# Kernel optimization log

Measured on AMD Instinct MI355X. Metric: run time of the kernel, lower is better.

The kernel has to match this reference:

```python
import jax, jax.numpy as jnp
import numpy as np
from jax import lax

B, C, H, W = 4, 512, 64, 64
C8 = C // 8
OUT = 256
BN_EPS = 1e-5


def setup_inputs() -> dict:
    key = jax.random.key(0)
    ks = jax.random.split(key, 12)
    s = lambda k, shape, fan: jax.random.normal(k, shape, jnp.float32) * (1.0 / np.sqrt(fan))
    return {
        "x": jax.random.normal(ks[0], (B, C, H, W), jnp.float32),
        "wq": s(ks[1], (C8, C), C), "bq": jnp.zeros((C8,), jnp.float32),
        "wk": s(ks[2], (C8, C), C), "bk": jnp.zeros((C8,), jnp.float32),
        "wv": s(ks[3], (C, C), C),  "bv": jnp.zeros((C,), jnp.float32),
        "ca_w1": s(ks[4], (C8, C), C),
        "ca_w2": s(ks[5], (C, C8), C8),
        "conv_w": s(ks[6], (OUT, C, 3, 3), C * 9),
        "bn_gamma": jnp.ones((OUT,), jnp.float32),
        "bn_beta": jnp.zeros((OUT,), jnp.float32),
        "bn_mean": jnp.zeros((OUT,), jnp.float32),
        "bn_var": jnp.ones((OUT,), jnp.float32),
    }


def reference(x, wq, bq, wk, bk, wv, bv, ca_w1, ca_w2, conv_w,
              bn_gamma, bn_beta, bn_mean, bn_var):
    b, c, h, w = x.shape
    n = h * w
    xf = x.reshape(b, c, n)  # [B,C,N]

    # ---- Position attention ----
    q = jnp.einsum('qc,bcn->bnq', wq, xf) + bq            # [B,N,C8]
    k = jnp.einsum('kc,bcn->bkn', wk, xf) + bk[:, None]   # [B,C8,N]
    energy = jnp.einsum('bnq,bqm->bnm', q, k)             # [B,N,N]
    attn = jax.nn.softmax(energy, axis=-1)
    v = jnp.einsum('vc,bcn->bvn', wv, xf) + bv[:, None]   # [B,C,N]
    # torch: bmm(value, attention^T) -> out[b,c,m] = sum_n v[b,c,n]*attn[b,m,n]
    pa = jnp.einsum('bcn,bmn->bcm', v, attn).reshape(b, c, h, w) + x

    # ---- Channel attention (SE-style, avg+max pooled, shared MLP) ----
    avg = jnp.mean(pa, axis=(2, 3))   # [B,C]
    mx = jnp.max(pa, axis=(2, 3))     # [B,C]
    fc = lambda z: jnp.einsum('oc,bc->bo', ca_w2,
                              jax.nn.relu(jnp.einsum('hc,bc->bh', ca_w1, z)))
    scale = jax.nn.sigmoid(fc(avg) + fc(mx))[:, :, None, None]
    ca = scale * pa

    # ---- Conv 3x3 + BN (eval mode) + ReLU ----
    y = lax.conv_general_dilated(ca, conv_w, (1, 1), 'SAME',
                                 dimension_numbers=('NCHW', 'OIHW', 'NCHW'))
    inv = lax.rsqrt(bn_var + BN_EPS)
    y = (y - bn_mean[:, None, None]) * (inv * bn_gamma)[:, None, None] + bn_beta[:, None, None]
    return jax.nn.relu(y)
```

## Files before the change

### kernel.cpp

```cpp
#include <hip/hip_runtime.h>

#define NB 4
#define CIN 512
#define NPIX 4096
#define CQK 64
#define COUT 256
#define PPIX 4356

typedef __bf16 bh16;
typedef _Float16 fh16;
typedef __attribute__((ext_vector_type(8))) __bf16 bf16x8;
typedef __attribute__((ext_vector_type(8))) _Float16 f16x8;
typedef __attribute__((ext_vector_type(16))) float f32x16;

#define AS1 __attribute__((address_space(1)))
#define AS3 __attribute__((address_space(3)))

__device__ __forceinline__ void glds16(const void* g, void* l) {
  __builtin_amdgcn_global_load_lds((const AS1 unsigned int*)g, (AS3 unsigned int*)l, 16, 0, 0);
}

__device__ __forceinline__ float fexp2(float x) {
#if __has_builtin(__builtin_amdgcn_exp2f)
  return __builtin_amdgcn_exp2f(x);
#else
  return __expf(x * 0.6931471805599453f);
#endif
}

__global__ __launch_bounds__(256) void transpose_bf_k(const float* __restrict__ src,
                                                      bh16* __restrict__ dst,
                                                      int rows, int cols) {
  __shared__ float tile[32][33];
  const int b = blockIdx.z;
  const int c0 = blockIdx.x * 32;
  const int r0 = blockIdx.y * 32;
  const float* s = src + (size_t)b * rows * cols;
  bh16* d = dst + (size_t)b * rows * cols;
  const int tx = threadIdx.x, ty = threadIdx.y;
#pragma unroll
  for (int i = 0; i < 32; i += 8)
    tile[ty + i][tx] = s[(size_t)(r0 + ty + i) * cols + (c0 + tx)];
  __syncthreads();
#pragma unroll
  for (int i = 0; i < 32; i += 8)
    d[(size_t)(c0 + ty + i) * rows + (r0 + tx)] = (bh16)tile[tx][ty + i];
}

__global__ __launch_bounds__(256) void wcast_k(const float* __restrict__ wq,
                                               const float* __restrict__ wk,
                                               const float* __restrict__ wv,
                                               const float* __restrict__ bq,
                                               const float* __restrict__ bk,
                                               bh16* __restrict__ Wqk,
                                               bh16* __restrict__ wvb,
                                               float* __restrict__ bias128) {
  const int idx = blockIdx.x * 256 + threadIdx.x;
  if (idx < 65536) {
    Wqk[idx] = (bh16)(idx < 32768 ? wq[idx] : wk[idx - 32768]);
  } else {
    const int j = idx - 65536;
    wvb[j] = (bh16)wv[j];
  }
  if (idx < 128) bias128[idx] = idx < 64 ? bq[idx] : bk[idx - 64];
}

__global__ __launch_bounds__(256) void qk_proj_k(const bh16* __restrict__ xTb,
                                                 const bh16* __restrict__ Wqk,
                                                 const float* __restrict__ bias128,
                                                 bh16* __restrict__ Qb,
                                                 bh16* __restrict__ Kf) {
  const int blk = blockIdx.x;
  const int t = threadIdx.x;
  const int w = t >> 6, l31 = t & 31, hi = (t & 63) >> 5;
  __shared__ __align__(16) bh16 As[2][64 * 64];
  f32x16 acc[2];
#pragma unroll
  for (int nt = 0; nt < 2; nt++)
#pragma unroll
    for (int r = 0; r < 16; r++) acc[nt][r] = 0.0f;

#define QK_STAGE(kc, buf)                                                           \
  {                                                                                 \
    _Pragma("unroll") for (int i = 0; i < 2; i++) {                                 \
      const int s = i * 256 + t;                                                    \
      const int n = s >> 3, slot = s & 7;                                           \
      glds16(xTb + (size_t)(blk * 64 + n) * CIN + (kc) * 64 + (((slot + n) & 7) * 8), \
             &As[buf][(size_t)(i * 256 + w * 64) * 8]);                             \
    }                                                                               \
  }

  QK_STAGE(0, 0);
  __syncthreads();
  for (int kc = 0; kc < 8; kc++) {
    if (kc < 7) QK_STAGE(kc + 1, (kc + 1) & 1);
    const bh16* as = As[kc & 1];
#pragma unroll
    for (int ks = 0; ks < 4; ks++) {
      const bf16x8 bfr = *(const bf16x8*)(Wqk + (size_t)(w * 32 + l31) * CIN + kc * 64 + ks * 16 + hi * 8);
      const int kk = ks * 2 + hi;
#pragma unroll
      for (int nt = 0; nt < 2; nt++) {
        const int n = nt * 32 + l31;
        const bf16x8 a = *(const bf16x8*)&as[(size_t)(n * 8 + ((kk - n) & 7)) * 8];
        acc[nt] = __builtin_amdgcn_mfma_f32_32x32x16_bf16(a, bfr, acc[nt], 0, 0, 0);
      }
    }
    __syncthreads();
  }
#undef QK_STAGE
  const int o = w * 32 + l31;
  const float bo = bias128[o];
  if (w < 2) {
#pragma unroll
    for (int nt = 0; nt < 2; nt++)
#pragma unroll
      for (int r = 0; r < 16; r++) {
        const int nloc = nt * 32 + (r & 3) + 8 * (r >> 2) + 4 * hi;
        Qb[(size_t)(blk * 64 + nloc) * 64 + o] = (bh16)((acc[nt][r] + bo) * 1.44269504088896f);
      }
  } else {
    const int b = blk >> 6, jtile = blk & 63;
    const int k = o - 64, kg = k >> 3, k7 = k & 7;
    bh16* kdst = Kf + (((size_t)(b * 64 + jtile) * 8 + kg) * 64) * 8 + k7;
#pragma unroll
    for (int nt = 0; nt < 2; nt++)
#pragma unroll
      for (int r = 0; r < 16; r++) {
        const int j = nt * 32 + (r & 3) + 8 * (r >> 2) + 4 * hi;
        kdst[(size_t)j * 8] = (bh16)(acc[nt][r] + bo);
      }
  }
}

__global__ __launch_bounds__(256) void v_proj_k(const bh16* __restrict__ xTb,
                                                const bh16* __restrict__ wvb,
                                                const float* __restrict__ bv,
                                                bh16* __restrict__ Vf) {
  const int nblk = blockIdx.x;
  const int cblk = blockIdx.y;
  const int b = blockIdx.z;
  const int t = threadIdx.x;
  const int w = t >> 6, l31 = t & 31, hi = (t & 63) >> 5;
  __shared__ __align__(16) bh16 Bs[2][256 * 64];
  f32x16 acc[2][2];
#pragma unroll
  for (int mt = 0; mt < 2; mt++)
#pragma unroll
    for (int nt = 0; nt < 2; nt++)
#pragma unroll
      for (int r = 0; r < 16; r++) acc[mt][nt][r] = 0.0f;

#define V_STAGE(kc, buf)                                                              \
  {                                                                                   \
    _Pragma("unroll") for (int i = 0; i < 8; i++) {                                   \
      const int s = i * 256 + t;                                                      \
      const int n = s >> 3, slot = s & 7;                                             \
      glds16(xTb + (size_t)(b * NPIX + nblk * 256 + n) * CIN + (kc) * 64 + (((slot + n) & 7) * 8), \
             &Bs[buf][(size_t)(i * 256 + w * 64) * 8]);                               \
    }                                                                                 \
  }

  V_STAGE(0, 0);
  __syncthreads();
  for (int kc = 0; kc < 8; kc++) {
    if (kc < 7) V_STAGE(kc + 1, (kc + 1) & 1);
    const bh16* bs = Bs[kc & 1];
#pragma unroll
    for (int ks = 0; ks < 4; ks++) {
      const int kk = ks * 2 + hi;
      bf16x8 a[2], bfr[2];
#pragma unroll
      for (int mt = 0; mt < 2; mt++)
        a[mt] = *(const bf16x8*)(wvb + (size_t)(cblk * 64 + mt * 32 + l31) * CIN + kc * 64 + ks * 16 + hi * 8);
#pragma unroll
      for (int nt = 0; nt < 2; nt++) {
        const int n = w * 64 + nt * 32 + l31;
        bfr[nt] = *(const bf16x8*)&bs[(size_t)(n * 8 + ((kk - n) & 7)) * 8];
      }
#pragma unroll
      for (int mt = 0; mt < 2; mt++)
#pragma unroll
        for (int nt = 0; nt < 2; nt++)
          acc[mt][nt] = __builtin_amdgcn_mfma_f32_32x32x16_bf16(a[mt], bfr[nt], acc[mt][nt], 0, 0, 0);
    }
    __syncthreads();
  }
#undef V_STAGE
  const int ntile0 = nblk * 4 + w;
#pragma unroll
  for (int mt = 0; mt < 2; mt++)
#pragma unroll
    for (int r = 0; r < 16; r++) {
      const int c = cblk * 64 + mt * 32 + (r & 3) + 8 * (r >> 2) + 4 * hi;
      const float bvc = bv[c];
#pragma unroll
      for (int nt = 0; nt < 2; nt++) {
        const int nl = nt * 32 + l31;
        Vf[(((size_t)(b * 64 + ntile0) * 8 + (nl >> 3)) * 512 + c) * 8 + (nl & 7)] =
            (bh16)(acc[mt][nt][r] + bvc);
      }
    }
}

__global__ __launch_bounds__(256, 2) void attn1p_k(const bh16* __restrict__ Qb,
                                                   const bh16* __restrict__ Kf,
                                                   const bh16* __restrict__ Vf,
                                                   const float* __restrict__ x,
                                                   float* __restrict__ pa) {
  const int id = blockIdx.x + 2 * (blockIdx.y + 64 * blockIdx.z);
  const int b = (id & 7) >> 1;
  const int cblk = id & 1;
  const int mblk = (id >> 3) * 64;
  const int t = threadIdx.x;
  const int w = t >> 6, l31 = t & 31, hi = (t >> 5) & 1;
  const int jhalf = w & 1, mhalf = w >> 1;
  __shared__ __align__(16) bh16 Ps[2][8 * 64 * 8];
  __shared__ float lred[4][32];
  __shared__ float linvL[64];

  bf16x8 qf[4];
  {
    const bh16* qrow = Qb + (size_t)(b * NPIX + mblk + mhalf * 32 + l31) * 64;
#pragma unroll
    for (int ks = 0; ks < 4; ks++) qf[ks] = *(const bf16x8*)(qrow + ks * 16 + hi * 8);
  }
  const bh16* kfb = Kf + (size_t)b * (64 * 8 * 64 * 8);
  const bh16* vfb = Vf + (size_t)b * (64 * 8 * 512 * 8);
  const int cbase = cblk * 256 + w * 64;

#define KADDR(tile, ks) (kfb + (((size_t)(tile) * 8 + (ks) * 2 + hi) * 64 + jhalf * 32 + l31) * 8)
#define VADDR(tile, ks, ct) (vfb + (((size_t)(tile) * 8 + (ks) * 2 + hi) * 512 + cbase + (ct) * 32 + l31) * 8)

  f32x16 acc[2][2];
#pragma unroll
  for (int mt = 0; mt < 2; mt++)
#pragma unroll
    for (int ct = 0; ct < 2; ct++)
#pragma unroll
      for (int r = 0; r < 16; r++) acc[mt][ct][r] = 0.0f;
  float4 lsacc;
  lsacc.x = 0.0f; lsacc.y = 0.0f; lsacc.z = 0.0f; lsacc.w = 0.0f;

  bf16x8 kf_nxt[4], kf_fly[4];
  bf16x8 vf_use[4][2], vf_rdy[4][2];
  f32x16 s1;
  {
    bf16x8 k0[4];
#pragma unroll
    for (int ks = 0; ks < 4; ks++) {
      k0[ks] = *(const bf16x8*)KADDR(0, ks);
#pragma unroll
      for (int ct = 0; ct < 2; ct++) vf_rdy[ks][ct] = *(const bf16x8*)VADDR(0, ks, ct);
    }
#pragma unroll
    for (int ks = 0; ks < 4; ks++) {
      kf_nxt[ks] = *(const bf16x8*)KADDR(1, ks);
      kf_fly[ks] = *(const bf16x8*)KADDR(2, ks);
    }
#pragma unroll
    for (int r = 0; r < 16; r++) s1[r] = 0.0f;
#pragma unroll
    for (int ks = 0; ks < 4; ks++)
      s1 = __builtin_amdgcn_mfma_f32_32x32x16_bf16(k0[ks], qf[ks], s1, 0, 0, 0);
  }

  for (int it = 0; it < 64; it++) {
    f32x16 s1n;
#pragma unroll
    for (int r = 0; r < 16; r++) s1n[r] = 0.0f;
#pragma unroll
    for (int ks = 0; ks < 4; ks++)
      s1n = __builtin_amdgcn_mfma_f32_32x32x16_bf16(kf_nxt[ks], qf[ks], s1n, 0, 0, 0);

    const bh16* ps = Ps[(it + 1) & 1];
    bh16* psw = Ps[it & 1];
    if (it) {
#pragma unroll
      for (int ks = 0; ks < 4; ks++) {
        bf16x8 pf0 = *(const bf16x8*)&ps[(size_t)((ks * 2 + hi) * 64 + l31) * 8];
        bf16x8 pf1 = *(const bf16x8*)&ps[(size_t)((ks * 2 + hi) * 64 + 32 + l31) * 8];
        acc[0][0] = __builtin_amdgcn_mfma_f32_32x32x16_bf16(pf0, vf_use[ks][0], acc[0][0], 0, 0, 0);
        acc[0][1] = __builtin_amdgcn_mfma_f32_32x32x16_bf16(pf0, vf_use[ks][1], acc[0][1], 0, 0, 0);
        {
          union { bh16 h[4]; uint2 u2; } pk;
#pragma unroll
          for (int q = 0; q < 4; q++) {
            const float p = fexp2(s1[ks * 4 + q]);
            lsacc[q] += p;
            pk.h[q] = (bh16)p;
          }
          *(uint2*)(void*)&psw[(size_t)((jhalf * 4 + ks) * 64 + mhalf * 32 + l31) * 8 + hi * 4] = pk.u2;
        }
        acc[1][0] = __builtin_amdgcn_mfma_f32_32x32x16_bf16(pf1, vf_use[ks][0], acc[1][0], 0, 0, 0);
        acc[1][1] = __builtin_amdgcn_mfma_f32_32x32x16_bf16(pf1, vf_use[ks][1], acc[1][1], 0, 0, 0);
      }
    } else {
#pragma unroll
      for (int g = 0; g < 4; g++) {
        union { bh16 h[4]; uint2 u2; } pk;
#pragma unroll
        for (int q = 0; q < 4; q++) {
          const float p = fexp2(s1[g * 4 + q]);
          lsacc[q] += p;
          pk.h[q] = (bh16)p;
        }
        *(uint2*)(void*)&psw[(size_t)((jhalf * 4 + g) * 64 + mhalf * 32 + l31) * 8 + hi * 4] = pk.u2;
      }
    }
    __syncthreads();
    s1 = s1n;
    const int kt = (it + 3 < 64) ? it + 3 : 63;
    const int vt = (it + 1 < 64) ? it + 1 : 63;
#pragma unroll
    for (int ks = 0; ks < 4; ks++) {
      kf_nxt[ks] = kf_fly[ks];
      kf_fly[ks] = *(const bf16x8*)KADDR(kt, ks);
      vf_use[ks][0] = vf_rdy[ks][0];
      vf_use[ks][1] = vf_rdy[ks][1];
      vf_rdy[ks][0] = *(const bf16x8*)VADDR(vt, ks, 0);
      vf_rdy[ks][1] = *(const bf16x8*)VADDR(vt, ks, 1);
    }
  }
  {
    const bh16* ps = Ps[1];
#pragma unroll
    for (int ks = 0; ks < 4; ks++) {
      bf16x8 pf0 = *(const bf16x8*)&ps[(size_t)((ks * 2 + hi) * 64 + l31) * 8];
      bf16x8 pf1 = *(const bf16x8*)&ps[(size_t)((ks * 2 + hi) * 64 + 32 + l31) * 8];
      acc[0][0] = __builtin_amdgcn_mfma_f32_32x32x16_bf16(pf0, vf_use[ks][0], acc[0][0], 0, 0, 0);
      acc[0][1] = __builtin_amdgcn_mfma_f32_32x32x16_bf16(pf0, vf_use[ks][1], acc[0][1], 0, 0, 0);
      acc[1][0] = __builtin_amdgcn_mfma_f32_32x32x16_bf16(pf1, vf_use[ks][0], acc[1][0], 0, 0, 0);
      acc[1][1] = __builtin_amdgcn_mfma_f32_32x32x16_bf16(pf1, vf_use[ks][1], acc[1][1], 0, 0, 0);
    }
  }
#undef KADDR
#undef VADDR

  float lsum = (lsacc.x + lsacc.y) + (lsacc.z + lsacc.w);
  lsum += __shfl_xor(lsum, 32);
  if (hi == 0) lred[w][l31] = lsum;
  __syncthreads();
  if (t < 64) linvL[t] = 1.0f / (lred[(t >> 5) * 2][t & 31] + lred[(t >> 5) * 2 + 1][t & 31]);
  __syncthreads();

#pragma unroll
  for (int mt = 0; mt < 2; mt++) {
#pragma unroll
    for (int g = 0; g < 4; g++) {
      const int mloc = mt * 32 + g * 8 + hi * 4;
      const float4 lv = *(const float4*)&linvL[mloc];
#pragma unroll
      for (int ct = 0; ct < 2; ct++) {
        const size_t base = (size_t)(b * CIN + cblk * 256 + w * 64 + ct * 32 + l31) * NPIX + mblk + mloc;
        const float4 xv = *(const float4*)&x[base];
        float4 r;
        r.x = acc[mt][ct][g * 4 + 0] * lv.x + xv.x;
        r.y = acc[mt][ct][g * 4 + 1] * lv.y + xv.y;
        r.z = acc[mt][ct][g * 4 + 2] * lv.z + xv.z;
        r.w = acc[mt][ct][g * 4 + 3] * lv.w + xv.w;
        *(float4*)&pa[base] = r;
      }
    }
  }
}

__global__ __launch_bounds__(256) void pool2_k(const float* __restrict__ pa,
                                               float* __restrict__ avgv,
                                               float* __restrict__ maxv) {
  const int t = threadIdx.x;
  const int row = blockIdx.x * 4 + (t >> 6);
  const int lane = t & 63;
  const float* base = pa + (size_t)row * NPIX;
  float s = 0.0f, mx = -1e30f;
#pragma unroll
  for (int i = 0; i < 16; i++) {
    const float4 v = *(const float4*)(base + i * 256 + lane * 4);
    s += v.x + v.y + v.z + v.w;
    mx = fmaxf(mx, fmaxf(fmaxf(v.x, v.y), fmaxf(v.z, v.w)));
  }
#pragma unroll
  for (int d = 1; d < 64; d <<= 1) {
    s += __shfl_xor(s, d);
    mx = fmaxf(mx, __shfl_xor(mx, d));
  }
  if (lane == 0) {
    avgv[row] = s * (1.0f / 4096.0f);
    maxv[row] = mx;
  }
}

__global__ __launch_bounds__(256) void mlp2_k(const float* __restrict__ avgv,
                                              const float* __restrict__ maxv,
                                              const float* __restrict__ w1,
                                              const float* __restrict__ w2,
                                              float* __restrict__ scale) {
  const int b = blockIdx.x;
  const int t = threadIdx.x;
  __shared__ float avg_l[CIN], max_l[CIN], hbuf[128];
#pragma unroll
  for (int h = 0; h < 2; h++) {
    const int c = t + h * 256;
    avg_l[c] = avgv[b * CIN + c];
    max_l[c] = maxv[b * CIN + c];
  }
  __syncthreads();
  if (t < 128) {
    const float* src = (t < 64) ? avg_l : max_l;
    const int o = t & 63;
    float sacc = 0.0f;
    for (int c = 0; c < CIN; c++) sacc += w1[o * CIN + c] * src[c];
    hbuf[t] = fmaxf(sacc, 0.0f);
  }
  __syncthreads();
#pragma unroll
  for (int h = 0; h < 2; h++) {
    const int c = t + h * 256;
    float sacc = 0.0f;
#pragma unroll
    for (int k = 0; k < 64; k++) sacc += w2[c * 64 + k] * (hbuf[k] + hbuf[64 + k]);
    scale[b * CIN + c] = 1.0f / (1.0f + __expf(-sacc));
  }
}

__global__ __launch_bounds__(256) void pack_k(const float* __restrict__ pa,
                                              const float* __restrict__ scl,
                                              fh16* __restrict__ pab) {
  __shared__ float tile[32][65];
  const int n0 = blockIdx.x * 32;
  const int c0 = blockIdx.y * 64;
  const int b = blockIdx.z;
  const int t = threadIdx.x;
  {
    const int px = t & 31, cc = t >> 5;
#pragma unroll
    for (int i = 0; i < 8; i++) {
      const int c = cc * 8 + i;
      tile[px][c] = pa[((size_t)(b * CIN + c0 + c)) * NPIX + n0 + px] * scl[b * CIN + c0 + c];
    }
  }
  __syncthreads();
  {
    const int pixr = t >> 5, c2 = (t & 31) * 2;
#pragma unroll
    for (int j = 0; j < 4; j++) {
      const int pix = pixr + j * 8;
      const int n = n0 + pix;
      const int pp = ((n >> 6) + 1) * 66 + (n & 63) + 1;
      union { fh16 h[2]; unsigned int u; } pk;
      pk.h[0] = (fh16)tile[pix][c2];
      pk.h[1] = (fh16)tile[pix][c2 + 1];
      *(unsigned int*)(void*)(pab + ((size_t)b * PPIX + pp) * CIN + c0 + c2) = pk.u;
    }
  }
}

__global__ __launch_bounds__(256) void bzero_k(fh16* __restrict__ pab) {
  const int t = threadIdx.x;
  const int p = blockIdx.x * 4 + (t >> 6);
  const int b = blockIdx.y;
  int pp;
  if (p < 66) pp = p;
  else if (p < 132) pp = 65 * 66 + (p - 66);
  else if (p < 196) pp = (p - 131) * 66;
  else pp = (p - 195) * 66 + 65;
  uint4 z = {0u, 0u, 0u, 0u};
  *(uint4*)(void*)(pab + ((size_t)b * PPIX + pp) * CIN + (t & 63) * 8) = z;
}

__global__ __launch_bounds__(256) void wpack_k(const float* __restrict__ cw,
                                               fh16* __restrict__ wp) {
  const int slot = blockIdx.x * 256 + threadIdx.x;
  const int oblk = slot / 36864;
  const int r1 = slot - oblk * 36864;
  const int chunk = r1 / 1152;
  const int r2 = r1 - chunk * 1152;
  const int tap = r2 >> 7;
  const int r3 = r2 & 127;
  const int h = r3 >> 6;
  const int o = r3 & 63;
  const size_t sbase = (size_t)(oblk * 64 + o) * 4608 + (size_t)(chunk * 16 + h * 8) * 9 + tap;
  union { fh16 h8[8]; uint4 u4; } pk;
#pragma unroll
  for (int i = 0; i < 8; i++) pk.h8[i] = (fh16)cw[sbase + (size_t)i * 9];
  *(uint4*)(void*)(wp + (size_t)slot * 8) = pk.u4;
}

__global__ __launch_bounds__(256) void conv_mfma_k(const fh16* __restrict__ pab,
                                                   const fh16* __restrict__ wp,
                                                   const float* __restrict__ gamma,
                                                   const float* __restrict__ beta,
                                                   const float* __restrict__ mean,
                                                   const float* __restrict__ var,
                                                   float* __restrict__ out) {
  const int y0 = blockIdx.x * 4;
  const int oblk = blockIdx.y;
  const int b = blockIdx.z;
  const int t = threadIdx.x;
  const int w = t >> 6, lane = t & 63, l31 = lane & 31, hi = lane >> 5;
  __shared__ __align__(16) fh16 Xs[2][416 * 16];
  __shared__ __align__(16) fh16 Ws[2][9 * 64 * 16];
  __shared__ float sb[64], bb[64];
  if (t < 64) {
    const int o = oblk * 64 + t;
    const float inv = rsqrtf(var[o] + 1e-5f);
    const float sc = inv * gamma[o];
    sb[t] = sc;
    bb[t] = beta[o] - mean[o] * sc;
  }
  f32x16 o00, o01, o10, o11;
#pragma unroll
  for (int r = 0; r < 16; r++) { o00[r] = 0.0f; o01[r] = 0.0f; o10[r] = 0.0f; o11[r] = 0.0f; }

  const fh16* xbase = pab + ((size_t)b * PPIX + y0 * 66) * CIN + (size_t)(lane & 31) * CIN + (lane >> 5) * 8;
  const fh16* wbase = wp + (size_t)oblk * 32 * 9216 + lane * 8;

#define STAGE(chunk, buf)                                                        \
  {                                                                              \
    const fh16* xs = xbase + (chunk) * 16;                                       \
    for (int i = w; i < 13; i += 4)                                              \
      glds16(xs + (size_t)i * 32 * CIN, &Xs[buf][i * 512]);                      \
    const fh16* wsrc = wbase + (size_t)(chunk) * 9216;                           \
    for (int i = w; i < 18; i += 4)                                              \
      glds16(wsrc + (size_t)i * 512, &Ws[buf][i * 512]);                         \
  }

  STAGE(0, 0);
  __syncthreads();
  for (int chunk = 0; chunk < 32; chunk++) {
    if (chunk < 31) STAGE(chunk + 1, (chunk + 1) & 1);
    const fh16* xs = Xs[chunk & 1];
    const fh16* ws = Ws[chunk & 1];
#pragma unroll
    for (int tap = 0; tap < 9; tap++) {
      const int ky = tap / 3, kx = tap - ky * 3;
      const f16x8 a0 = *(const f16x8*)&ws[tap * 1024 + hi * 512 + l31 * 8];
      const f16x8 a1 = *(const f16x8*)&ws[tap * 1024 + hi * 512 + (32 + l31) * 8];
      const int row0 = (w + ky) * 66 + l31 + kx;
      const int row1 = row0 + 32;
      const f16x8 b0 = *(const f16x8*)&xs[(row0 >> 5) * 512 + hi * 256 + (row0 & 31) * 8];
      const f16x8 b1 = *(const f16x8*)&xs[(row1 >> 5) * 512 + hi * 256 + (row1 & 31) * 8];
      o00 = __builtin_amdgcn_mfma_f32_32x32x16_f16(a0, b0, o00, 0, 0, 0);
      o01 = __builtin_amdgcn_mfma_f32_32x32x16_f16(a0, b1, o01, 0, 0, 0);
      o10 = __builtin_amdgcn_mfma_f32_32x32x16_f16(a1, b0, o10, 0, 0, 0);
      o11 = __builtin_amdgcn_mfma_f32_32x32x16_f16(a1, b1, o11, 0, 0, 0);
    }
    __syncthreads();
  }
#undef STAGE

  const f32x16* accs[2][2] = {{&o00, &o01}, {&o10, &o11}};
#pragma unroll
  for (int mt = 0; mt < 2; mt++) {
#pragma unroll
    for (int nt = 0; nt < 2; nt++) {
      const f32x16& A = *accs[mt][nt];
#pragma unroll
      for (int r = 0; r < 16; r++) {
        const int cl = mt * 32 + (r & 3) + 8 * (r >> 2) + 4 * hi;
        const int pix = nt * 32 + l31;
        const float y = A[r] * sb[cl] + bb[cl];
        out[((size_t)(b * COUT + oblk * 64 + cl)) * NPIX + (y0 + w) * 64 + pix] = fmaxf(y, 0.0f);
      }
    }
  }
}

extern "C" void kernel_launch(void* const* d_in, const int* in_sizes, int n_in,
                              void* d_out, int out_size, void* d_ws, size_t ws_size,
                              hipStream_t stream) {
  (void)in_sizes; (void)n_in; (void)out_size; (void)ws_size;
  const float* x        = (const float*)d_in[0];
  const float* wq       = (const float*)d_in[1];
  const float* bq       = (const float*)d_in[2];
  const float* wk       = (const float*)d_in[3];
  const float* bk       = (const float*)d_in[4];
  const float* wv       = (const float*)d_in[5];
  const float* bv       = (const float*)d_in[6];
  const float* ca_w1    = (const float*)d_in[7];
  const float* ca_w2    = (const float*)d_in[8];
  const float* conv_w   = (const float*)d_in[9];
  const float* bn_gamma = (const float*)d_in[10];
  const float* bn_beta  = (const float*)d_in[11];
  const float* bn_mean  = (const float*)d_in[12];
  const float* bn_var   = (const float*)d_in[13];
  float* out = (float*)d_out;

  float* ws = (float*)d_ws;
  float* pa      = ws;
  bh16*  Vf      = (bh16*)(ws + 8388608);
  fh16*  wpck    = (fh16*)(ws + 8388608);
  bh16*  Qb      = (bh16*)(ws + 12582912);
  bh16*  Kf      = (bh16*)(ws + 13107200);
  bh16*  xTb     = (bh16*)(ws + 13631488);
  fh16*  pab     = (fh16*)(ws + 13631488);
  bh16*  Wqk     = (bh16*)(ws + 17825792);
  bh16*  wvb     = (bh16*)(ws + 17858560);
  float* bias128 = ws + 17989632;
  float* avgv    = ws + 18100224;
  float* maxv    = ws + 18102272;
  float* scl     = ws + 18104320;

  wcast_k<<<dim3(1280, 1, 1), 256, 0, stream>>>(wq, wk, wv, bq, bk, Wqk, wvb, bias128);
  transpose_bf_k<<<dim3(NPIX / 32, CIN / 32, NB), dim3(32, 8, 1), 0, stream>>>(x, xTb, CIN, NPIX);
  qk_proj_k<<<dim3(256, 1, 1), 256, 0, stream>>>(xTb, Wqk, bias128, Qb, Kf);
  v_proj_k<<<dim3(16, 8, NB), 256, 0, stream>>>(xTb, wvb, bv, Vf);
  attn1p_k<<<dim3(2, 64, NB), 256, 0, stream>>>(Qb, Kf, Vf, x, pa);
  bzero_k<<<dim3(65, NB, 1), 256, 0, stream>>>(pab);
  pool2_k<<<dim3(512, 1, 1), 256, 0, stream>>>(pa, avgv, maxv);
  mlp2_k<<<dim3(NB, 1, 1), 256, 0, stream>>>(avgv, maxv, ca_w1, ca_w2, scl);
  pack_k<<<dim3(NPIX / 32, CIN / 64, NB), 256, 0, stream>>>(pa, scl, pab);
  wpack_k<<<dim3(576, 1, 1), 256, 0, stream>>>(conv_w, wpck);
  conv_mfma_k<<<dim3(16, 4, NB), 256, 0, stream>>>(pab, wpck, bn_gamma, bn_beta,
                                                   bn_mean, bn_var, out);
}
```

Measured before the change: 335.3 us.

## Fuse channel pooling into attention epilogue and store pa as fp16 NHWC

The attention kernel now writes pa as fp16 in pixel-major (NHWC) layout and computes per-block partial sums and maxima per channel. This removes the separate pool2 kernel, and the MLP kernel reduces the 64 partials instead. The pack kernel becomes a simple scaled copy with no shared-memory transpose. The K/V prefetch pipeline is also made shallower to lower register pressure. In exchange, the epilogue now issues scattered 2-byte stores, and the pre-scale activation is rounded to fp16.

```diff
diff --git a/kernel.cpp b/kernel.cpp
--- a/kernel.cpp
+++ b/kernel.cpp
@@ -207,7 +207,9 @@
                                                    const bh16* __restrict__ Kf,
                                                    const bh16* __restrict__ Vf,
                                                    const float* __restrict__ x,
-                                                   float* __restrict__ pa) {
+                                                   fh16* __restrict__ pa,
+                                                   float* __restrict__ psum,
+                                                   float* __restrict__ pmax) {
   const int id = blockIdx.x + 2 * (blockIdx.y + 64 * blockIdx.z);
   const int b = (id & 7) >> 1;
   const int cblk = id & 1;
@@ -242,8 +244,8 @@
   float4 lsacc;
   lsacc.x = 0.0f; lsacc.y = 0.0f; lsacc.z = 0.0f; lsacc.w = 0.0f;
 
-  bf16x8 kf_nxt[4], kf_fly[4];
-  bf16x8 vf_use[4][2], vf_rdy[4][2];
+  bf16x8 kf_nxt[4];
+  bf16x8 vf_use[4][2];
   f32x16 s1;
   {
     bf16x8 k0[4];
@@ -251,13 +253,10 @@
     for (int ks = 0; ks < 4; ks++) {
       k0[ks] = *(const bf16x8*)KADDR(0, ks);
 #pragma unroll
-      for (int ct = 0; ct < 2; ct++) vf_rdy[ks][ct] = *(const bf16x8*)VADDR(0, ks, ct);
-    }
-#pragma unroll
-    for (int ks = 0; ks < 4; ks++) {
-      kf_nxt[ks] = *(const bf16x8*)KADDR(1, ks);
-      kf_fly[ks] = *(const bf16x8*)KADDR(2, ks);
-    }
+      for (int ct = 0; ct < 2; ct++) vf_use[ks][ct] = *(const bf16x8*)VADDR(0, ks, ct);
+    }
+#pragma unroll
+    for (int ks = 0; ks < 4; ks++) kf_nxt[ks] = *(const bf16x8*)KADDR(1, ks);
 #pragma unroll
     for (int r = 0; r < 16; r++) s1[r] = 0.0f;
 #pragma unroll
@@ -272,6 +271,11 @@
 #pragma unroll
     for (int ks = 0; ks < 4; ks++)
       s1n = __builtin_amdgcn_mfma_f32_32x32x16_bf16(kf_nxt[ks], qf[ks], s1n, 0, 0, 0);
+    {
+      const int kt = (it + 2 < 64) ? it + 2 : 63;
+#pragma unroll
+      for (int ks = 0; ks < 4; ks++) kf_nxt[ks] = *(const bf16x8*)KADDR(kt, ks);
+    }
 
     const bh16* ps = Ps[(it + 1) & 1];
     bh16* psw = Ps[it & 1];
@@ -294,6 +298,8 @@
         }
         acc[1][0] = __builtin_amdgcn_mfma_f32_32x32x16_bf16(pf1, vf_use[ks][0], acc[1][0], 0, 0, 0);
         acc[1][1] = __builtin_amdgcn_mfma_f32_32x32x16_bf16(pf1, vf_use[ks][1], acc[1][1], 0, 0, 0);
+        vf_use[ks][0] = *(const bf16x8*)VADDR(it, ks, 0);
+        vf_use[ks][1] = *(const bf16x8*)VADDR(it, ks, 1);
       }
     } else {
 #pragma unroll
@@ -310,17 +316,6 @@
     }
     __syncthreads();
     s1 = s1n;
-    const int kt = (it + 3 < 64) ? it + 3 : 63;
-    const int vt = (it + 1 < 64) ? it + 1 : 63;
-#pragma unroll
-    for (int ks = 0; ks < 4; ks++) {
-      kf_nxt[ks] = kf_fly[ks];
-      kf_fly[ks] = *(const bf16x8*)KADDR(kt, ks);
-      vf_use[ks][0] = vf_rdy[ks][0];
-      vf_use[ks][1] = vf_rdy[ks][1];
-      vf_rdy[ks][0] = *(const bf16x8*)VADDR(vt, ks, 0);
-      vf_rdy[ks][1] = *(const bf16x8*)VADDR(vt, ks, 1);
-    }
   }
   {
     const bh16* ps = Ps[1];
@@ -344,6 +339,8 @@
   if (t < 64) linvL[t] = 1.0f / (lred[(t >> 5) * 2][t & 31] + lred[(t >> 5) * 2 + 1][t & 31]);
   __syncthreads();
 
+  float csum[2] = {0.0f, 0.0f};
+  float cmax[2] = {-1e30f, -1e30f};
 #pragma unroll
   for (int mt = 0; mt < 2; mt++) {
 #pragma unroll
@@ -352,46 +349,40 @@
       const float4 lv = *(const float4*)&linvL[mloc];
 #pragma unroll
       for (int ct = 0; ct < 2; ct++) {
-        const size_t base = (size_t)(b * CIN + cblk * 256 + w * 64 + ct * 32 + l31) * NPIX + mblk + mloc;
-        const float4 xv = *(const float4*)&x[base];
-        float4 r;
-        r.x = acc[mt][ct][g * 4 + 0] * lv.x + xv.x;
-        r.y = acc[mt][ct][g * 4 + 1] * lv.y + xv.y;
-        r.z = acc[mt][ct][g * 4 + 2] * lv.z + xv.z;
-        r.w = acc[mt][ct][g * 4 + 3] * lv.w + xv.w;
-        *(float4*)&pa[base] = r;
-      }
-    }
-  }
-}
-
-__global__ __launch_bounds__(256) void pool2_k(const float* __restrict__ pa,
-                                               float* __restrict__ avgv,
-                                               float* __restrict__ maxv) {
-  const int t = threadIdx.x;
-  const int row = blockIdx.x * 4 + (t >> 6);
-  const int lane = t & 63;
-  const float* base = pa + (size_t)row * NPIX;
-  float s = 0.0f, mx = -1e30f;
-#pragma unroll
-  for (int i = 0; i < 16; i++) {
-    const float4 v = *(const float4*)(base + i * 256 + lane * 4);
-    s += v.x + v.y + v.z + v.w;
-    mx = fmaxf(mx, fmaxf(fmaxf(v.x, v.y), fmaxf(v.z, v.w)));
-  }
-#pragma unroll
-  for (int d = 1; d < 64; d <<= 1) {
-    s += __shfl_xor(s, d);
-    mx = fmaxf(mx, __shfl_xor(mx, d));
-  }
-  if (lane == 0) {
-    avgv[row] = s * (1.0f / 4096.0f);
-    maxv[row] = mx;
-  }
-}
-
-__global__ __launch_bounds__(256) void mlp2_k(const float* __restrict__ avgv,
-                                              const float* __restrict__ maxv,
+        const int c = cbase + ct * 32 + l31;
+        const float4 xv = *(const float4*)&x[(size_t)(b * CIN + c) * NPIX + mblk + mloc];
+        float r0 = acc[mt][ct][g * 4 + 0] * lv.x + xv.x;
+        float r1 = acc[mt][ct][g * 4 + 1] * lv.y + xv.y;
+        float r2 = acc[mt][ct][g * 4 + 2] * lv.z + xv.z;
+        float r3 = acc[mt][ct][g * 4 + 3] * lv.w + xv.w;
+        csum[ct] += (r0 + r1) + (r2 + r3);
+        cmax[ct] = fmaxf(cmax[ct], fmaxf(fmaxf(r0, r1), fmaxf(r2, r3)));
+        fh16* pd = pa + ((size_t)(b * NPIX) + mblk + mloc) * CIN + c;
+        pd[0 * CIN] = (fh16)r0;
+        pd[1 * CIN] = (fh16)r1;
+        pd[2 * CIN] = (fh16)r2;
+        pd[3 * CIN] = (fh16)r3;
+      }
+    }
+  }
+#pragma unroll
+  for (int ct = 0; ct < 2; ct++) {
+    csum[ct] += __shfl_xor(csum[ct], 32);
+    cmax[ct] = fmaxf(cmax[ct], __shfl_xor(cmax[ct], 32));
+  }
+  if (hi == 0) {
+    const int mb = mblk >> 6;
+#pragma unroll
+    for (int ct = 0; ct < 2; ct++) {
+      const int c = cbase + ct * 32 + l31;
+      psum[((size_t)b * 64 + mb) * CIN + c] = csum[ct];
+      pmax[((size_t)b * 64 + mb) * CIN + c] = cmax[ct];
+    }
+  }
+}
+
+__global__ __launch_bounds__(256) void mlp2_k(const float* __restrict__ psum,
+                                              const float* __restrict__ pmax,
                                               const float* __restrict__ w1,
                                               const float* __restrict__ w2,
                                               float* __restrict__ scale) {
@@ -401,8 +392,14 @@
 #pragma unroll
   for (int h = 0; h < 2; h++) {
     const int c = t + h * 256;
-    avg_l[c] = avgv[b * CIN + c];
-    max_l[c] = maxv[b * CIN + c];
+    float s = 0.0f, m = -1e30f;
+#pragma unroll
+    for (int k = 0; k < 64; k++) {
+      s += psum[((size_t)b * 64 + k) * CIN + c];
+      m = fmaxf(m, pmax[((size_t)b * 64 + k) * CIN + c]);
+    }
+    avg_l[c] = s * (1.0f / 4096.0f);
+    max_l[c] = m;
   }
   __syncthreads();
   if (t < 128) {
@@ -423,35 +420,27 @@
   }
 }
 
-__global__ __launch_bounds__(256) void pack_k(const float* __restrict__ pa,
+__global__ __launch_bounds__(256) void pack_k(const fh16* __restrict__ pa,
                                               const float* __restrict__ scl,
                                               fh16* __restrict__ pab) {
-  __shared__ float tile[32][65];
-  const int n0 = blockIdx.x * 32;
-  const int c0 = blockIdx.y * 64;
-  const int b = blockIdx.z;
+  const int b = blockIdx.y;
+  const int n0 = blockIdx.x * 8;
   const int t = threadIdx.x;
-  {
-    const int px = t & 31, cc = t >> 5;
-#pragma unroll
-    for (int i = 0; i < 8; i++) {
-      const int c = cc * 8 + i;
-      tile[px][c] = pa[((size_t)(b * CIN + c0 + c)) * NPIX + n0 + px] * scl[b * CIN + c0 + c];
-    }
-  }
-  __syncthreads();
-  {
-    const int pixr = t >> 5, c2 = (t & 31) * 2;
-#pragma unroll
-    for (int j = 0; j < 4; j++) {
-      const int pix = pixr + j * 8;
-      const int n = n0 + pix;
-      const int pp = ((n >> 6) + 1) * 66 + (n & 63) + 1;
-      union { fh16 h[2]; unsigned int u; } pk;
-      pk.h[0] = (fh16)tile[pix][c2];
-      pk.h[1] = (fh16)tile[pix][c2 + 1];
-      *(unsigned int*)(void*)(pab + ((size_t)b * PPIX + pp) * CIN + c0 + c2) = pk.u;
-    }
+  __shared__ float sc[CIN];
+#pragma unroll
+  for (int h = 0; h < 2; h++) sc[t + h * 256] = scl[b * CIN + t + h * 256];
+  __syncthreads();
+  const int c2 = t * 2;
+  const float s0 = sc[c2], s1 = sc[c2 + 1];
+#pragma unroll
+  for (int j = 0; j < 8; j++) {
+    const int n = n0 + j;
+    const int pp = ((n >> 6) + 1) * 66 + (n & 63) + 1;
+    union { fh16 h[2]; unsigned int u; } v, o;
+    v.u = *(const unsigned int*)(pa + ((size_t)b * NPIX + n) * CIN + c2);
+    o.h[0] = (fh16)((float)v.h[0] * s0);
+    o.h[1] = (fh16)((float)v.h[1] * s1);
+    *(unsigned int*)(void*)(pab + ((size_t)b * PPIX + pp) * CIN + c2) = o.u;
   }
 }
 
@@ -587,7 +576,9 @@
   float* out = (float*)d_out;
 
   float* ws = (float*)d_ws;
-  float* pa      = ws;
+  fh16*  pa      = (fh16*)ws;
+  float* psum    = ws + 4194304;
+  float* pmax    = ws + 4325376;
   bh16*  Vf      = (bh16*)(ws + 8388608);
   fh16*  wpck    = (fh16*)(ws + 8388608);
   bh16*  Qb      = (bh16*)(ws + 12582912);
@@ -597,19 +588,16 @@
   bh16*  Wqk     = (bh16*)(ws + 17825792);
   bh16*  wvb     = (bh16*)(ws + 17858560);
   float* bias128 = ws + 17989632;
-  float* avgv    = ws + 18100224;
-  float* maxv    = ws + 18102272;
   float* scl     = ws + 18104320;
 
   wcast_k<<<dim3(1280, 1, 1), 256, 0, stream>>>(wq, wk, wv, bq, bk, Wqk, wvb, bias128);
   transpose_bf_k<<<dim3(NPIX / 32, CIN / 32, NB), dim3(32, 8, 1), 0, stream>>>(x, xTb, CIN, NPIX);
   qk_proj_k<<<dim3(256, 1, 1), 256, 0, stream>>>(xTb, Wqk, bias128, Qb, Kf);
   v_proj_k<<<dim3(16, 8, NB), 256, 0, stream>>>(xTb, wvb, bv, Vf);
-  attn1p_k<<<dim3(2, 64, NB), 256, 0, stream>>>(Qb, Kf, Vf, x, pa);
+  attn1p_k<<<dim3(2, 64, NB), 256, 0, stream>>>(Qb, Kf, Vf, x, pa, psum, pmax);
   bzero_k<<<dim3(65, NB, 1), 256, 0, stream>>>(pab);
-  pool2_k<<<dim3(512, 1, 1), 256, 0, stream>>>(pa, avgv, maxv);
-  mlp2_k<<<dim3(NB, 1, 1), 256, 0, stream>>>(avgv, maxv, ca_w1, ca_w2, scl);
-  pack_k<<<dim3(NPIX / 32, CIN / 64, NB), 256, 0, stream>>>(pa, scl, pab);
+  mlp2_k<<<dim3(NB, 1, 1), 256, 0, stream>>>(psum, pmax, ca_w1, ca_w2, scl);
+  pack_k<<<dim3(NPIX / 8, NB, 1), 256, 0, stream>>>(pa, scl, pab);
   wpack_k<<<dim3(576, 1, 1), 256, 0, stream>>>(conv_w, wpck);
   conv_mfma_k<<<dim3(16, 4, NB), 256, 0, stream>>>(pab, wpck, bn_gamma, bn_beta,
                                                    bn_mean, bn_var, out);
```

Result: faster. 320.6 us (-4.4%).
